# Optimization experiments

Measured on AMD Instinct MI355X. Metric: run time of the kernel, lower is better.

Reference implementation:

```python
import math
import jax, jax.numpy as jnp
import numpy as np

N, C, H, W = 4096, 64, 16, 16
E = 16
CAP_FACTOR = 1.5  # eval-mode capacity factor in the torch source
CCAP = max(1, math.ceil(CAP_FACTOR * N / E))  # 384


def setup_inputs() -> dict:
    key = jax.random.key(0)
    k1, k2 = jax.random.split(key)
    X = jax.random.normal(k1, (N, C, H, W), dtype=jnp.float32)
    W_gate = jax.random.normal(k2, (C, E), dtype=jnp.float32) * 0.1
    b_gate = jnp.zeros((E,), dtype=jnp.float32)
    return {"X": X, "W_gate": W_gate, "b_gate": b_gate}


def reference(X, W_gate, b_gate):
    # router_gate: global average pool over spatial dims + linear -> [N, E]
    pooled = X.mean(axis=(2, 3))                       # [N, C]
    logits = pooled @ W_gate + b_gate                  # [N, E]

    # z-loss: mean logsumexp over experts
    z_loss = jnp.mean(jax.nn.logsumexp(logits, axis=-1))

    # eval path (not training): softmax over experts, top-1
    probs = jax.nn.softmax(logits.astype(jnp.float32), axis=1)  # [N, E]
    expert_gate = probs.max(axis=1)                    # [N]
    expert_index = jnp.argmax(probs, axis=1)           # [N]
    expert_mask = jax.nn.one_hot(expert_index, E, dtype=probs.dtype)  # [N, E]

    # aux (load-balance) loss computed BEFORE capacity masking, as in source
    density_1 = expert_mask.mean(axis=0)
    density_2 = probs.mean(axis=0)
    aux_loss = jnp.sum(density_1 * density_2) * E

    # capacity-constrained position via cumsum over tokens
    position_in_exp = jnp.cumsum(expert_mask, axis=0) - 1.0   # [N, E]
    within_capacity = (position_in_exp < CCAP).astype(probs.dtype)
    expert_mask = expert_mask * within_capacity
    expert_mask_flat = expert_mask.sum(axis=-1)               # [N]
    expert_gate = expert_gate * expert_mask_flat

    pos_idx = jnp.clip(position_in_exp, 0, CCAP - 1).astype(jnp.int32)  # [N, E]
    one_hot_pos = jax.nn.one_hot(pos_idx, CCAP, dtype=probs.dtype)      # [N, E, Ccap]

    combine = (expert_gate[:, None, None] * expert_mask[:, :, None] * one_hot_pos).astype(X.dtype)
    dispatch = combine > 0
    return dispatch, combine, z_loss, aux_loss
```

## Files before the change

kernel.cpp:

```cpp
#include <hip/hip_runtime.h>
#include <math.h>

#define N_TOK 4096
#define C_CH  64
#define HW    256
#define E_EXP 16
#define CCAP  384
#define NEC   (N_TOK * E_EXP * CCAP)


__global__ __launch_bounds__(256) void k_zero(float* __restrict__ out, float* __restrict__ ws) {
    float4* o4 = (float4*)out;
    const long long n4 = (2LL * NEC) / 4;
    long long i = (long long)blockIdx.x * blockDim.x + threadIdx.x;
    const long long stride = (long long)gridDim.x * blockDim.x;
    const float4 z = {0.f, 0.f, 0.f, 0.f};
    for (; i < n4; i += stride) o4[i] = z;
    if (blockIdx.x == 0) {
        for (int j = threadIdx.x; j < 1088; j += blockDim.x) ws[j] = 0.f;
    }
}

__global__ __launch_bounds__(256) void k_router(const float* __restrict__ X,
                                                const float* __restrict__ Wg,
                                                const float* __restrict__ bg,
                                                float* __restrict__ ws) {
    __shared__ float Wl[C_CH * E_EXP];
    __shared__ float waveacc[4][E_EXP];

    const int t = threadIdx.x;
    const int n = blockIdx.x;
    for (int j = t; j < C_CH * E_EXP; j += 256) Wl[j] = Wg[j];
    __syncthreads();

    const int w = t >> 6, lane = t & 63;
    const float4* Xv = (const float4*)(X + (long long)n * (C_CH * HW));

    float acc[E_EXP];
#pragma unroll
    for (int e = 0; e < E_EXP; ++e) acc[e] = 0.f;

#pragma unroll
    for (int k = 0; k < 16; ++k) {
        float4 v = Xv[k * 256 + w * 64 + lane];
        float s = (v.x + v.y) + (v.z + v.w);
        const int c = k * 4 + w;
#pragma unroll
        for (int e = 0; e < E_EXP; ++e) acc[e] = fmaf(s, Wl[c * E_EXP + e], acc[e]);
    }

#pragma unroll
    for (int off = 32; off > 0; off >>= 1) {
#pragma unroll
        for (int e = 0; e < E_EXP; ++e) acc[e] += __shfl_xor(acc[e], off, 64);
    }
    if (lane == 0) {
#pragma unroll
        for (int e = 0; e < E_EXP; ++e) waveacc[w][e] = acc[e];
    }
    __syncthreads();

    if (t < E_EXP) {
        const int e = t;
        float logit = (waveacc[0][e] + waveacc[1][e] + waveacc[2][e] + waveacc[3][e]) * (1.f / HW)
                      + bg[e];
        float m = logit;
#pragma unroll
        for (int off = 8; off > 0; off >>= 1) m = fmaxf(m, __shfl_xor(m, off, 16));
        float ex = expf(logit - m);
        float s = ex;
#pragma unroll
        for (int off = 8; off > 0; off >>= 1) s += __shfl_xor(s, off, 16);
        int aidx = (logit == m) ? e : 1000;
#pragma unroll
        for (int off = 8; off > 0; off >>= 1) aidx = min(aidx, __shfl_xor(aidx, off, 16));

        const float prob = ex / s;
        atomicAdd(&ws[64 + e * 64 + (n & 63)], prob);
        if (e == 0) {
            atomicAdd(&ws[n & 63], m + logf(s));
            ws[1088 + n] = 1.f / s;
            ((int*)ws)[5184 + n] = aidx;
        }
    }
}

__global__ __launch_bounds__(256) void k_scan(float* __restrict__ out, float* __restrict__ ws) {
    __shared__ int cnt[256 * 17];
    __shared__ int run[256 * 17];
    const int t = threadIdx.x;
    const int* idx = (const int*)ws + 5184;
    const float* gate = ws + 1088;

#pragma unroll
    for (int e = 0; e < 17; ++e) cnt[t * 17 + e] = 0;
    const int n0 = t * 16;
    for (int j = 0; j < 16; ++j) cnt[t * 17 + idx[n0 + j]]++;
    __syncthreads();

    for (int step = 1; step < 256; step <<= 1) {
        int v[E_EXP];
        if (t >= step) {
#pragma unroll
            for (int e = 0; e < E_EXP; ++e) v[e] = cnt[(t - step) * 17 + e];
        }
        __syncthreads();
        if (t >= step) {
#pragma unroll
            for (int e = 0; e < E_EXP; ++e) cnt[t * 17 + e] += v[e];
        }
        __syncthreads();
    }

#pragma unroll
    for (int e = 0; e < E_EXP; ++e) run[t * 17 + e] = (t == 0) ? 0 : cnt[(t - 1) * 17 + e];
    __syncthreads();

    for (int j = 0; j < 16; ++j) {
        const int n = n0 + j;
        const int e = idx[n];
        const int pos = run[t * 17 + e]++;
        if (pos < CCAP) {
            const long long col = (long long)n * (E_EXP * CCAP) + e * CCAP + pos;
            out[col] = 1.0f;
            out[NEC + col] = gate[n];
        }
    }

    if (t == 0) {
        float zs = 0.f;
        for (int j = 0; j < 64; ++j) zs += ws[j];
        float aux = 0.f;
        for (int e = 0; e < E_EXP; ++e) {
            float ps = 0.f;
            for (int j = 0; j < 64; ++j) ps += ws[64 + e * 64 + j];
            const float d1 = (float)cnt[255 * 17 + e] / (float)N_TOK;
            aux += d1 * (ps / (float)N_TOK);
        }
        out[2LL * NEC]     = zs / (float)N_TOK;
        out[2LL * NEC + 1] = aux * (float)E_EXP;
    }
}

extern "C" void kernel_launch(void* const* d_in, const int* in_sizes, int n_in,
                              void* d_out, int out_size, void* d_ws, size_t ws_size,
                              hipStream_t stream) {
    const float* X  = (const float*)d_in[0];
    const float* Wg = (const float*)d_in[1];
    const float* bg = (const float*)d_in[2];
    float* out = (float*)d_out;
    float* ws  = (float*)d_ws;

    hipLaunchKernelGGL(k_zero,   dim3(2048), dim3(256), 0, stream, out, ws);
    hipLaunchKernelGGL(k_router, dim3(N_TOK), dim3(256), 0, stream, X, Wg, bg, ws);
    hipLaunchKernelGGL(k_scan,   dim3(1),    dim3(256), 0, stream, out, ws);
}
```

Before: 470.7 us.

## Fuse output zeroing into router kernel and replace atomics with per-token workspace

The separate zero-fill kernel is removed. Each router block now clears its own token's slice of the dispatch/combine output with nontemporal vector stores, so the zero writes overlap with the reads of X. The per-token probabilities and logsumexp values are written to plain workspace slots instead of being atomically added into 64 shared bins. The single-block scan kernel then reduces them with wave shuffles, which removes atomic contention and the workspace clearing. The cost is more serial reduction work inside the one-block scan kernel.

```diff
diff --git a/kernel.cpp b/kernel.cpp
--- a/kernel.cpp
+++ b/kernel.cpp
@@ -2,43 +2,39 @@
 #include <math.h>
 
 #define N_TOK 4096
-#define C_CH  64
-#define HW    256
 #define E_EXP 16
 #define CCAP  384
 #define NEC   (N_TOK * E_EXP * CCAP)
 
+typedef float floatx4 __attribute__((ext_vector_type(4)));
 
-__global__ __launch_bounds__(256) void k_zero(float* __restrict__ out, float* __restrict__ ws) {
-    float4* o4 = (float4*)out;
-    const long long n4 = (2LL * NEC) / 4;
-    long long i = (long long)blockIdx.x * blockDim.x + threadIdx.x;
-    const long long stride = (long long)gridDim.x * blockDim.x;
-    const float4 z = {0.f, 0.f, 0.f, 0.f};
-    for (; i < n4; i += stride) o4[i] = z;
-    if (blockIdx.x == 0) {
-        for (int j = threadIdx.x; j < 1088; j += blockDim.x) ws[j] = 0.f;
-    }
-}
 
-__global__ __launch_bounds__(256) void k_router(const float* __restrict__ X,
-                                                const float* __restrict__ Wg,
-                                                const float* __restrict__ bg,
-                                                float* __restrict__ ws) {
-    __shared__ float Wl[C_CH * E_EXP];
-    __shared__ float waveacc[4][E_EXP];
-
+__global__ __launch_bounds__(256) void k_main(const float* __restrict__ X,
+                                              const float* __restrict__ Wg,
+                                              const float* __restrict__ bg,
+                                              float* __restrict__ out,
+                                              float* __restrict__ ws) {
+    __shared__ float Wl[64 * 16];
+    __shared__ float waveacc[4][16];
     const int t = threadIdx.x;
     const int n = blockIdx.x;
-    for (int j = t; j < C_CH * E_EXP; j += 256) Wl[j] = Wg[j];
+
+    {
+        floatx4* o4 = (floatx4*)out + (long long)n * 3072 + t;
+        const floatx4 z = {0.f, 0.f, 0.f, 0.f};
+#pragma unroll
+        for (int j = 0; j < 12; ++j) __builtin_nontemporal_store(z, o4 + j * 256);
+    }
+
+    for (int j = t; j < 64 * 16; j += 256) Wl[j] = Wg[j];
     __syncthreads();
 
     const int w = t >> 6, lane = t & 63;
-    const float4* Xv = (const float4*)(X + (long long)n * (C_CH * HW));
+    const float4* Xv = (const float4*)(X + (long long)n * 16384);
 
-    float acc[E_EXP];
+    float acc[16];
 #pragma unroll
-    for (int e = 0; e < E_EXP; ++e) acc[e] = 0.f;
+    for (int e = 0; e < 16; ++e) acc[e] = 0.f;
 
 #pragma unroll
     for (int k = 0; k < 16; ++k) {
@@ -46,23 +42,23 @@
         float s = (v.x + v.y) + (v.z + v.w);
         const int c = k * 4 + w;
 #pragma unroll
-        for (int e = 0; e < E_EXP; ++e) acc[e] = fmaf(s, Wl[c * E_EXP + e], acc[e]);
+        for (int e = 0; e < 16; ++e) acc[e] = fmaf(s, Wl[c * 16 + e], acc[e]);
     }
 
 #pragma unroll
     for (int off = 32; off > 0; off >>= 1) {
 #pragma unroll
-        for (int e = 0; e < E_EXP; ++e) acc[e] += __shfl_xor(acc[e], off, 64);
+        for (int e = 0; e < 16; ++e) acc[e] += __shfl_xor(acc[e], off, 64);
     }
     if (lane == 0) {
 #pragma unroll
-        for (int e = 0; e < E_EXP; ++e) waveacc[w][e] = acc[e];
+        for (int e = 0; e < 16; ++e) waveacc[w][e] = acc[e];
     }
     __syncthreads();
 
-    if (t < E_EXP) {
+    if (t < 16) {
         const int e = t;
-        float logit = (waveacc[0][e] + waveacc[1][e] + waveacc[2][e] + waveacc[3][e]) * (1.f / HW)
+        float logit = (waveacc[0][e] + waveacc[1][e] + waveacc[2][e] + waveacc[3][e]) * (1.f / 256.f)
                       + bg[e];
         float m = logit;
 #pragma unroll
@@ -75,12 +71,11 @@
 #pragma unroll
         for (int off = 8; off > 0; off >>= 1) aidx = min(aidx, __shfl_xor(aidx, off, 16));
 
-        const float prob = ex / s;
-        atomicAdd(&ws[64 + e * 64 + (n & 63)], prob);
+        ws[12288 + n * 16 + e] = ex / s;
         if (e == 0) {
-            atomicAdd(&ws[n & 63], m + logf(s));
-            ws[1088 + n] = 1.f / s;
-            ((int*)ws)[5184 + n] = aidx;
+            ws[n] = 1.f / s;
+            ((int*)ws)[4096 + n] = aidx;
+            ws[8192 + n] = m + logf(s);
         }
     }
 }
@@ -88,32 +83,64 @@
 __global__ __launch_bounds__(256) void k_scan(float* __restrict__ out, float* __restrict__ ws) {
     __shared__ int cnt[256 * 17];
     __shared__ int run[256 * 17];
+    __shared__ float wred[4][17];
     const int t = threadIdx.x;
-    const int* idx = (const int*)ws + 5184;
-    const float* gate = ws + 1088;
+    const int* idx = (const int*)ws + 4096;
+    const float* gate = ws;
+    const float* lse = ws + 8192;
+    const float4* pv = (const float4*)(ws + 12288);
+    const int n0 = t * 16;
+
+    float zp = 0.f;
+    float pp[16];
+#pragma unroll
+    for (int e = 0; e < 16; ++e) pp[e] = 0.f;
+    for (int j = 0; j < 16; ++j) {
+        const int n = n0 + j;
+        zp += lse[n];
+#pragma unroll
+        for (int q = 0; q < 4; ++q) {
+            float4 v = pv[n * 4 + q];
+            pp[q * 4 + 0] += v.x; pp[q * 4 + 1] += v.y;
+            pp[q * 4 + 2] += v.z; pp[q * 4 + 3] += v.w;
+        }
+    }
+    {
+        const int w = t >> 6, lane = t & 63;
+#pragma unroll
+        for (int off = 32; off > 0; off >>= 1) {
+            zp += __shfl_xor(zp, off, 64);
+#pragma unroll
+            for (int e = 0; e < 16; ++e) pp[e] += __shfl_xor(pp[e], off, 64);
+        }
+        if (lane == 0) {
+            wred[w][16] = zp;
+#pragma unroll
+            for (int e = 0; e < 16; ++e) wred[w][e] = pp[e];
+        }
+    }
 
 #pragma unroll
     for (int e = 0; e < 17; ++e) cnt[t * 17 + e] = 0;
-    const int n0 = t * 16;
     for (int j = 0; j < 16; ++j) cnt[t * 17 + idx[n0 + j]]++;
     __syncthreads();
 
     for (int step = 1; step < 256; step <<= 1) {
-        int v[E_EXP];
+        int v[16];
         if (t >= step) {
 #pragma unroll
-            for (int e = 0; e < E_EXP; ++e) v[e] = cnt[(t - step) * 17 + e];
+            for (int e = 0; e < 16; ++e) v[e] = cnt[(t - step) * 17 + e];
         }
         __syncthreads();
         if (t >= step) {
 #pragma unroll
-            for (int e = 0; e < E_EXP; ++e) cnt[t * 17 + e] += v[e];
+            for (int e = 0; e < 16; ++e) cnt[t * 17 + e] += v[e];
         }
         __syncthreads();
     }
 
 #pragma unroll
-    for (int e = 0; e < E_EXP; ++e) run[t * 17 + e] = (t == 0) ? 0 : cnt[(t - 1) * 17 + e];
+    for (int e = 0; e < 16; ++e) run[t * 17 + e] = (t == 0) ? 0 : cnt[(t - 1) * 17 + e];
     __syncthreads();
 
     for (int j = 0; j < 16; ++j) {
@@ -128,12 +155,10 @@
     }
 
     if (t == 0) {
-        float zs = 0.f;
-        for (int j = 0; j < 64; ++j) zs += ws[j];
+        float zs = wred[0][16] + wred[1][16] + wred[2][16] + wred[3][16];
         float aux = 0.f;
-        for (int e = 0; e < E_EXP; ++e) {
-            float ps = 0.f;
-            for (int j = 0; j < 64; ++j) ps += ws[64 + e * 64 + j];
+        for (int e = 0; e < 16; ++e) {
+            const float ps = wred[0][e] + wred[1][e] + wred[2][e] + wred[3][e];
             const float d1 = (float)cnt[255 * 17 + e] / (float)N_TOK;
             aux += d1 * (ps / (float)N_TOK);
         }
@@ -151,7 +176,6 @@
     float* out = (float*)d_out;
     float* ws  = (float*)d_ws;
 
-    hipLaunchKernelGGL(k_zero,   dim3(2048), dim3(256), 0, stream, out, ws);
-    hipLaunchKernelGGL(k_router, dim3(N_TOK), dim3(256), 0, stream, X, Wg, bg, ws);
-    hipLaunchKernelGGL(k_scan,   dim3(1),    dim3(256), 0, stream, out, ws);
+    hipLaunchKernelGGL(k_main, dim3(N_TOK), dim3(256), 0, stream, X, Wg, bg, out, ws);
+    hipLaunchKernelGGL(k_scan, dim3(1),     dim3(256), 0, stream, out, ws);
 }
```

New measurement: 455.8 us. -3.2%, faster.
